# Kernel tuning notes

Hardware: AMD Instinct MI355X
Metric: run time of the kernel (lower is better)

## Reference

```python
import jax, jax.numpy as jnp
import numpy as np
from jax import lax

B, N, C = 16, 2000, 81
MAX_INST = 100
MIN_CONF = 0.7
NMS_THR = 0.3
BBOX_STD = jnp.array([0.1, 0.1, 0.2, 0.2], jnp.float32)
IMG_H = IMG_W = 1024
NEG = -1e9


def setup_inputs() -> dict:
    key = jax.random.key(0)
    k1, k2, k3 = jax.random.split(key, 3)
    # rois: normalized boxes with y1<y2, x1<x2
    yx = jax.random.uniform(k1, (B, N, 2, 2), dtype=jnp.float32)
    y = jnp.sort(yx[..., 0], axis=-1)
    x = jnp.sort(yx[..., 1], axis=-1)
    rois = jnp.stack([y[..., 0], x[..., 0], y[..., 1], x[..., 1]], axis=-1)
    # class probabilities (softmax over classes); temperature makes some scores pass 0.7
    mrcnn_class = jax.nn.softmax(3.0 * jax.random.normal(k2, (B, N, C), dtype=jnp.float32), axis=-1)
    mrcnn_bbox = 0.1 * jax.random.normal(k3, (B, N, C, 4), dtype=jnp.float32)
    # image_meta: [image_id(1), original_shape(3), image_shape(3), window(4), scale(1), active_class_ids(C)]
    meta = np.zeros((B, 12 + C), np.float32)
    meta[:, 1:4] = [IMG_H, IMG_W, 3]
    meta[:, 4:7] = [IMG_H, IMG_W, 3]
    meta[:, 7:11] = [0, 0, IMG_H, IMG_W]
    meta[:, 11] = 1.0
    return {"rois": rois, "mrcnn_class": mrcnn_class, "mrcnn_bbox": mrcnn_bbox,
            "image_meta": jnp.asarray(meta)}


def _apply_deltas(boxes, deltas):
    h = boxes[:, 2] - boxes[:, 0]
    w = boxes[:, 3] - boxes[:, 1]
    cy = boxes[:, 0] + 0.5 * h
    cx = boxes[:, 1] + 0.5 * w
    cy = cy + deltas[:, 0] * h
    cx = cx + deltas[:, 1] * w
    h = h * jnp.exp(deltas[:, 2])
    w = w * jnp.exp(deltas[:, 3])
    return jnp.stack([cy - 0.5 * h, cx - 0.5 * w, cy + 0.5 * h, cx + 0.5 * w], axis=-1)


def _iou_row(box, boxes):
    y1 = jnp.maximum(box[0], boxes[:, 0])
    x1 = jnp.maximum(box[1], boxes[:, 1])
    y2 = jnp.minimum(box[2], boxes[:, 2])
    x2 = jnp.minimum(box[3], boxes[:, 3])
    inter = jnp.maximum(y2 - y1, 0.0) * jnp.maximum(x2 - x1, 0.0)
    a1 = (box[2] - box[0]) * (box[3] - box[1])
    a2 = (boxes[:, 2] - boxes[:, 0]) * (boxes[:, 3] - boxes[:, 1])
    return inter / (a1 + a2 - inter + 1e-12)


def _refine_one(rois, probs, deltas, window):
    # rois [N,4], probs [N,C], deltas [N,C,4], window [4]
    idx = jnp.arange(N)
    class_ids = jnp.argmax(probs, axis=1)                 # [N]
    scores = probs[idx, class_ids]                        # [N]
    d = deltas[idx, class_ids] * BBOX_STD                 # [N,4]
    boxes = _apply_deltas(rois, d)
    wy1, wx1, wy2, wx2 = window[0], window[1], window[2], window[3]
    boxes = jnp.stack([jnp.clip(boxes[:, 0], wy1, wy2),
                       jnp.clip(boxes[:, 1], wx1, wx2),
                       jnp.clip(boxes[:, 2], wy1, wy2),
                       jnp.clip(boxes[:, 3], wx1, wx2)], axis=-1)
    # filter background and low confidence
    kept = (class_ids > 0) & (scores >= MIN_CONF)
    masked_scores = jnp.where(kept, scores, NEG)
    order = jnp.argsort(-masked_scores)                   # descending by score
    b = boxes[order]
    c = class_ids[order]
    s = masked_scores[order]
    suppressed0 = ~kept[order]

    def body(i, sup):
        iou = _iou_row(b[i], b)                           # [N]
        kill = (iou > NMS_THR) & (c == c[i]) & (idx > i) & (~sup[i])
        return sup | kill

    sup = lax.fori_loop(0, N, body, suppressed0)          # class-wise greedy NMS
    final = jnp.where(sup, NEG, s)
    top_s, top_i = lax.top_k(final, MAX_INST)             # global top detections
    det = jnp.concatenate([b[top_i],
                           c[top_i, None].astype(jnp.float32),
                           top_s[:, None]], axis=-1)      # [MAX_INST, 6]
    valid = top_s >= MIN_CONF
    return jnp.where(valid[:, None], det, 0.0)            # zero-pad invalid rows


def reference(rois, mrcnn_class, mrcnn_bbox, image_meta):
    image_shape = image_meta[0, 4:7]
    window = image_meta[:, 7:11]                          # [B,4] in pixels
    h, w = image_shape[0], image_shape[1]
    scale = jnp.stack([h - 1.0, w - 1.0, h - 1.0, w - 1.0])
    shift = jnp.array([0.0, 0.0, 1.0, 1.0], jnp.float32)
    norm_window = (window - shift) / scale                # norm_boxes_graph
    dets = jax.vmap(_refine_one)(rois, mrcnn_class, mrcnn_bbox, norm_window)
    return dets.reshape(B, MAX_INST, 6)
```

## Files before the change

### kernel.cpp

```cpp
#include <hip/hip_runtime.h>

#define NB    16
#define NN    2000
#define NC    81
#define NPAD  2048
#define MAXI  100
#define MINC  0.7f
#define NMST  0.3f
#define NEGV  -1000000000.0f
#define BTP   256
#define BT    1024
#define NWAVE (BT/64)
#define KQ    ((NN + BT - 1) / BT)

#define WS_BOX_OFF  0
#define WS_KEY_OFF  (NB * NN * 16)
#define WS_NEEDED   (WS_KEY_OFF + NB * NN * 8)

__device__ __forceinline__ unsigned ordf(float f) {
    unsigned u = __float_as_uint(f);
    return (u & 0x80000000u) ? ~u : (u | 0x80000000u);
}
__device__ __forceinline__ float unordf(unsigned u) {
    unsigned b = (u & 0x80000000u) ? (u ^ 0x80000000u) : ~u;
    return __uint_as_float(b);
}

__device__ __forceinline__ unsigned long long cx64(unsigned long long k, int j,
                                                   bool desc, int lane) {
    unsigned lo = __shfl_xor((unsigned)k, j, 64);
    unsigned hi = __shfl_xor((unsigned)(k >> 32), j, 64);
    unsigned long long p = ((unsigned long long)hi << 32) | lo;
    bool lower    = ((lane & j) == 0);
    bool take_max = (lower == desc);
    return ((p > k) == take_max) ? p : k;
}


__global__ __launch_bounds__(BTP)
void prep_kernel(const float* __restrict__ rois,
                 const float* __restrict__ probs,
                 const float* __restrict__ deltas,
                 const float* __restrict__ meta,
                 float4* __restrict__ wbox,
                 unsigned long long* __restrict__ wkey) {
    const int g = threadIdx.x >> 4;
    const int l = threadIdx.x & 15;
    const int r = blockIdx.x * 16 + g;
    const int b = r / NN;
    const int i = r - b * NN;

    const float* prow = probs + (size_t)r * NC;
    float best = -1.0f; int cb = 0;
    for (int c = l; c < NC; c += 16) {
        float p = prow[c];
        if (p > best) { best = p; cb = c; }
    }
    #pragma unroll
    for (int off = 8; off; off >>= 1) {
        float pb = __shfl_xor(best, off, 16);
        int   co = __shfl_xor(cb,   off, 16);
        if (pb > best || (pb == best && co < cb)) { best = pb; cb = co; }
    }

    if (l == 0) {
        const int MS = 12 + NC;
        const float ih = meta[4], iw = meta[5];
        const float sy = ih - 1.0f, sx = iw - 1.0f;
        const float wy1 = (meta[(size_t)b * MS + 7]        ) / sy;
        const float wx1 = (meta[(size_t)b * MS + 8]        ) / sx;
        const float wy2 = (meta[(size_t)b * MS + 9]  - 1.0f) / sy;
        const float wx2 = (meta[(size_t)b * MS + 10] - 1.0f) / sx;

        const float* drow = deltas + ((size_t)r * NC + cb) * 4;
        float dy = drow[0] * 0.1f, dx = drow[1] * 0.1f;
        float dh = drow[2] * 0.2f, dw = drow[3] * 0.2f;

        const float4 r4 = *(const float4*)(rois + (size_t)r * 4);
        float h  = r4.z - r4.x;
        float w  = r4.w - r4.y;
        float cy = r4.x + 0.5f * h;
        float cx = r4.y + 0.5f * w;
        cy = cy + dy * h;
        cx = cx + dx * w;
        h  = h * expf(dh);
        w  = w * expf(dw);
        float y1 = fminf(fmaxf(cy - 0.5f * h, wy1), wy2);
        float x1 = fminf(fmaxf(cx - 0.5f * w, wx1), wx2);
        float y2 = fminf(fmaxf(cy + 0.5f * h, wy1), wy2);
        float x2 = fminf(fmaxf(cx + 0.5f * w, wx1), wx2);

        wbox[r] = make_float4(y1, x1, y2, x2);
        bool kept = (cb > 0) && (best >= MINC);
        float msc = kept ? best : NEGV;
        wkey[r] = ((unsigned long long)ordf(msc) << 32)
                | (unsigned long long)(((unsigned)(2047 - i) << 8) | (unsigned)cb);
    }
}

__global__ __launch_bounds__(BT)
void det2_kernel(const float4* __restrict__ wbox,
                 const unsigned long long* __restrict__ wkey,
                 float* __restrict__ out) {
    __shared__ unsigned long long skey[NPAD];
    __shared__ float4 sboxR[NPAD];
    __shared__ unsigned char sup[NPAD];
    __shared__ unsigned short pool[NPAD];
    __shared__ int hist[82], cstart[82], cnt[82];
    __shared__ int out_rank[MAXI];
    __shared__ int sK, nsurv;

    const int b    = blockIdx.x;
    const int tid  = threadIdx.x;
    const int lane = tid & 63;
    const int wv   = tid >> 6;

    for (int c = tid; c < 82; c += BT) { hist[c] = 0; cnt[c] = 0; }
    if (tid == 0) { sK = 0; nsurv = 0; }
    __syncthreads();

    const unsigned minc_ord = ordf(MINC);
    unsigned long long kq[KQ];
    #pragma unroll
    for (int q = 0; q < KQ; ++q) {
        int i = q * BT + tid;
        kq[q] = (i < NN) ? wkey[(size_t)b * NN + i] : 0ull;
    }
    #pragma unroll
    for (int q = 0; q < KQ; ++q) {
        bool kept = ((unsigned)(kq[q] >> 32) >= minc_ord);
        unsigned long long m = __ballot(kept);
        int c64 = __popcll(m);
        int basep = 0;
        if (lane == 0 && c64) basep = atomicAdd(&sK, c64);
        basep = __shfl(basep, 0, 64);
        if (kept) skey[basep + __popcll(m & ((1ull << lane) - 1))] = kq[q];
    }
    __syncthreads();
    const int K = sK;
    int P = 0;
    if (K > 0) { P = 64; while (P < K) P <<= 1; }
    for (int t = K + tid; t < P; t += BT) skey[t] = 0ull;
    __syncthreads();

    if (P > 0 && P <= 64 * NWAVE) {
        const int nch = P >> 6;
        const int e   = (wv << 6) + lane;
        unsigned long long k = 0ull;
        if (wv < nch) {
            k = skey[e];
            #pragma unroll
            for (int kk2 = 2; kk2 <= 64; kk2 <<= 1) {
                #pragma unroll
                for (int j = 32; j; j >>= 1) {
                    if (j < kk2) k = cx64(k, j, ((e & kk2) == 0), lane);
                }
            }
            skey[e] = k;
        }
        __syncthreads();
        for (int kk = 128; kk <= P; kk <<= 1) {
            for (int j = kk >> 1; j >= 64; j >>= 1) {
                int jm = j - 1;
                for (int p = tid; p < (P >> 1); p += BT) {
                    int t  = ((p & ~jm) << 1) | (p & jm);
                    int ix = t + j;
                    unsigned long long a = skey[t], c2 = skey[ix];
                    bool desc = ((t & kk) == 0);
                    if ((a < c2) == desc) { skey[t] = c2; skey[ix] = a; }
                }
                __syncthreads();
            }
            if (wv < nch) {
                k = skey[e];
                const bool desc = ((e & kk) == 0);
                #pragma unroll
                for (int j = 32; j; j >>= 1) k = cx64(k, j, desc, lane);
                skey[e] = k;
            }
            __syncthreads();
        }
    } else if (P > 0) {
        for (int kk = 2; kk <= P; kk <<= 1) {
            for (int j = kk >> 1; j > 0; j >>= 1) {
                int jm = j - 1;
                for (int p = tid; p < (P >> 1); p += BT) {
                    int t  = ((p & ~jm) << 1) | (p & jm);
                    int ix = t + j;
                    unsigned long long a = skey[t], c2 = skey[ix];
                    bool desc = ((t & kk) == 0);
                    if ((a < c2) == desc) { skey[t] = c2; skey[ix] = a; }
                }
                __syncthreads();
            }
        }
    }

    for (int r2 = tid; r2 < K; r2 += BT) {
        unsigned low = (unsigned)(skey[r2] & 0xFFFFFFFFull);
        int oi = 2047 - (int)((low >> 8) & 0x7FF);
        sboxR[r2] = wbox[(size_t)b * NN + oi];
        sup[r2] = 0;
        atomicAdd(&hist[low & 0xFF], 1);
    }
    __syncthreads();

    if (wv == 0) {
        int c0 = 2 * lane, c1 = c0 + 1;
        int h0 = (c0 < 82) ? hist[c0] : 0;
        int h1 = (c1 < 82) ? hist[c1] : 0;
        int s = h0 + h1, sc = s;
        #pragma unroll
        for (int off = 1; off < 64; off <<= 1) {
            int v = __shfl_up(sc, off, 64);
            if (lane >= off) sc += v;
        }
        int excl = sc - s;
        if (c0 < 82) cstart[c0] = excl;
        if (c1 < 82) cstart[c1] = excl + h0;
    }
    __syncthreads();

    if (wv == 0) {
        for (int chunk = 0; chunk < K; chunk += 64) {
            int r2 = chunk + lane;
            bool v = r2 < K;
            int c = v ? (int)(skey[r2] & 0xFF) : 127;
            unsigned long long m = ~0ull;
            #pragma unroll
            for (int kb = 0; kb < 7; ++kb) {
                unsigned long long bk = __ballot((c >> kb) & 1);
                m &= ((c >> kb) & 1) ? bk : ~bk;
            }
            int leader = __ffsll(m) - 1;
            int before = __popcll(m & ((1ull << lane) - 1));
            int basec = 0;
            if (v && lane == leader) basec = atomicAdd(&cnt[c], __popcll(m));
            basec = __shfl(basec, leader, 64);
            if (v) pool[cstart[c] + basec + before] = (unsigned short)r2;
        }
    }
    __syncthreads();

    for (int c = 1 + wv; c < 82; c += NWAVE) {
        int s0 = cstart[c], n = hist[c];
        if (n <= 1) continue;
        if (n <= 64) {
            int ri = 0; float4 bi = make_float4(0.f,0.f,0.f,0.f);
            float ai = 0.f; bool alive = false;
            if (lane < n) {
                ri = pool[s0 + lane];
                bi = sboxR[ri];
                ai = (bi.z - bi.x) * (bi.w - bi.y);
                alive = true;
            }
            unsigned long long cand = __ballot(alive);
            while (cand) {
                int curl = __ffsll(cand) - 1;
                float cy1 = __shfl(bi.x, curl, 64);
                float cx1 = __shfl(bi.y, curl, 64);
                float cy2 = __shfl(bi.z, curl, 64);
                float cx2 = __shfl(bi.w, curl, 64);
                float ca  = __shfl(ai,  curl, 64);
                float yy1 = fmaxf(cy1, bi.x);
                float xx1 = fmaxf(cx1, bi.y);
                float yy2 = fminf(cy2, bi.z);
                float xx2 = fminf(cx2, bi.w);
                float inter = fmaxf(yy2 - yy1, 0.0f) * fmaxf(xx2 - xx1, 0.0f);
                float iou = inter / (ca + ai - inter + 1e-12f);
                bool kill = alive && (lane > curl) && (iou > NMST);
                unsigned long long km = __ballot(kill);
                if (kill) alive = false;
                cand &= ~km;
                cand &= ~(1ull << curl);
            }
            if (lane < n && !alive) sup[ri] = 1;
        } else {
            volatile unsigned char* vsup = sup;
            for (int ii = 0; ii < n; ++ii) {
                int ri = pool[s0 + ii];
                if (vsup[ri]) continue;
                float4 bi = sboxR[ri];
                float ai = (bi.z - bi.x) * (bi.w - bi.y);
                for (int jj = ii + 1 + lane; jj < n; jj += 64) {
                    int rj = pool[s0 + jj];
                    float4 bj = sboxR[rj];
                    float yy1 = fmaxf(bi.x, bj.x);
                    float xx1 = fmaxf(bi.y, bj.y);
                    float yy2 = fminf(bi.z, bj.z);
                    float xx2 = fminf(bi.w, bj.w);
                    float inter = fmaxf(yy2 - yy1, 0.0f) * fmaxf(xx2 - xx1, 0.0f);
                    float aj = (bj.z - bj.x) * (bj.w - bj.y);
                    float iou = inter / (ai + aj - inter + 1e-12f);
                    if (iou > NMST) vsup[rj] = 1;
                }
            }
        }
    }
    __syncthreads();

    if (wv == 0) {
        int total = 0;
        for (int chunk = 0; chunk < K && total < MAXI; chunk += 64) {
            int r2 = chunk + lane;
            bool alivex = (r2 < K) && !sup[r2];
            unsigned long long m = __ballot(alivex);
            int pos = total + __popcll(m & ((1ull << lane) - 1));
            if (alivex && pos < MAXI) out_rank[pos] = r2;
            total += __popcll(m);
        }
        if (lane == 0) nsurv = total < MAXI ? total : MAXI;
    }
    __syncthreads();

    const int ns = nsurv;
    for (int o = tid; o < MAXI; o += BT) {
        float v0=0.f,v1=0.f,v2=0.f,v3=0.f,v4=0.f,v5=0.f;
        if (o < ns) {
            int r2 = out_rank[o];
            float4 bo = sboxR[r2];
            unsigned long long kr = skey[r2];
            v0 = bo.x; v1 = bo.y; v2 = bo.z; v3 = bo.w;
            v4 = (float)(int)(kr & 0xFF);
            v5 = unordf((unsigned)(kr >> 32));
        }
        float* op = out + ((size_t)b * MAXI + o) * 6;
        op[0]=v0; op[1]=v1; op[2]=v2; op[3]=v3; op[4]=v4; op[5]=v5;
    }
}

__global__ __launch_bounds__(256)
void det_mono_kernel(const float* __restrict__ rois,
                     const float* __restrict__ probs,
                     const float* __restrict__ deltas,
                     const float* __restrict__ meta,
                     float* __restrict__ out) {
    __shared__ unsigned long long key[NPAD];
    __shared__ float4 sbox[NN];
    __shared__ unsigned char scls[NN];
    __shared__ unsigned char sup[NPAD];
    __shared__ int out_rank[MAXI];
    __shared__ int sK;
    __shared__ int nsurv;

    const int b   = blockIdx.x;
    const int tid = threadIdx.x;
    const int MSTRIDE = 12 + NC;

    if (tid == 0) { sK = 0; nsurv = 0; }

    const float ih = meta[4], iw = meta[5];
    const float sy = ih - 1.0f, sx = iw - 1.0f;
    const float wy1 = (meta[(size_t)b * MSTRIDE + 7]) / sy;
    const float wx1 = (meta[(size_t)b * MSTRIDE + 8]) / sx;
    const float wy2 = (meta[(size_t)b * MSTRIDE + 9] - 1.0f) / sy;
    const float wx2 = (meta[(size_t)b * MSTRIDE + 10] - 1.0f) / sx;

    for (int i = tid; i < NN; i += 256) {
        const float* prow = probs + ((size_t)b * NN + i) * NC;
        float best = prow[0];
        int cb = 0;
        #pragma unroll
        for (int c = 1; c < NC; ++c) {
            float p = prow[c];
            if (p > best) { best = p; cb = c; }
        }
        const float* drow = deltas + (((size_t)b * NN + i) * NC + cb) * 4;
        float dy = drow[0] * 0.1f, dx = drow[1] * 0.1f;
        float dh = drow[2] * 0.2f, dw = drow[3] * 0.2f;
        const float4 r4 = *(const float4*)(rois + ((size_t)b * NN + i) * 4);
        float h  = r4.z - r4.x;
        float w  = r4.w - r4.y;
        float cy = r4.x + 0.5f * h;
        float cx = r4.y + 0.5f * w;
        cy = cy + dy * h;
        cx = cx + dx * w;
        h  = h * expf(dh);
        w  = w * expf(dw);
        float y1 = fminf(fmaxf(cy - 0.5f * h, wy1), wy2);
        float x1 = fminf(fmaxf(cx - 0.5f * w, wx1), wx2);
        float y2 = fminf(fmaxf(cy + 0.5f * h, wy1), wy2);
        float x2 = fminf(fmaxf(cx + 0.5f * w, wx1), wx2);
        sbox[i] = make_float4(y1, x1, y2, x2);
        scls[i] = (unsigned char)cb;
        bool kept = (cb > 0) && (best >= MINC);
        float msc = kept ? best : NEGV;
        key[i] = ((unsigned long long)ordf(msc) << 32)
               | (unsigned long long)(0xFFFFFFFFu - (unsigned)i);
    }
    for (int i = NN + tid; i < NPAD; i += 256) key[i] = 0ull;
    __syncthreads();

    for (int k = 2; k <= NPAD; k <<= 1) {
        for (int j = k >> 1; j > 0; j >>= 1) {
            for (int t = tid; t < NPAD; t += 256) {
                int ix = t ^ j;
                if (ix > t) {
                    unsigned long long a = key[t], c = key[ix];
                    bool descend = ((t & k) == 0);
                    if ((a < c) == descend) { key[t] = c; key[ix] = a; }
                }
            }
            __syncthreads();
        }
    }

    const unsigned minc_ord = ordf(MINC);
    for (int r = tid; r < NPAD; r += 256) {
        unsigned su = (unsigned)(key[r] >> 32);
        bool kept = (su >= minc_ord);
        sup[r] = kept ? 0 : 1;
        if (kept) atomicAdd(&sK, 1);
    }
    __syncthreads();
    const int K = sK;

    for (int i = 0; i < K; ++i) {
        __syncthreads();
        if (nsurv >= MAXI) break;
        if (sup[i]) continue;
        unsigned long long ki = key[i];
        int oi = (int)(0xFFFFFFFFu - (unsigned)(ki & 0xFFFFFFFFull));
        float4 bi = sbox[oi];
        int ci = scls[oi];
        float ai = (bi.z - bi.x) * (bi.w - bi.y);
        for (int jr = i + 1 + tid; jr < K; jr += 256) {
            int oj = (int)(0xFFFFFFFFu - (unsigned)(key[jr] & 0xFFFFFFFFull));
            if ((int)scls[oj] != ci) continue;
            float4 bj = sbox[oj];
            float yy1 = fmaxf(bi.x, bj.x);
            float xx1 = fmaxf(bi.y, bj.y);
            float yy2 = fminf(bi.z, bj.z);
            float xx2 = fminf(bi.w, bj.w);
            float inter = fmaxf(yy2 - yy1, 0.0f) * fmaxf(xx2 - xx1, 0.0f);
            float aj = (bj.z - bj.x) * (bj.w - bj.y);
            float iou = inter / (ai + aj - inter + 1e-12f);
            if (iou > NMST) sup[jr] = 1;
        }
        if (tid == 0) { out_rank[nsurv] = i; nsurv += 1; }
    }
    __syncthreads();

    const int ns = nsurv;
    for (int o = tid; o < MAXI; o += 256) {
        float v0=0.f,v1=0.f,v2=0.f,v3=0.f,v4=0.f,v5=0.f;
        if (o < ns) {
            int r = out_rank[o];
            unsigned long long kr = key[r];
            int orr = (int)(0xFFFFFFFFu - (unsigned)(kr & 0xFFFFFFFFull));
            float4 bo = sbox[orr];
            v0 = bo.x; v1 = bo.y; v2 = bo.z; v3 = bo.w;
            v4 = (float)scls[orr];
            v5 = unordf((unsigned)(kr >> 32));
        }
        float* op = out + ((size_t)b * MAXI + o) * 6;
        op[0]=v0; op[1]=v1; op[2]=v2; op[3]=v3; op[4]=v4; op[5]=v5;
    }
}

extern "C" void kernel_launch(void* const* d_in, const int* in_sizes, int n_in,
                              void* d_out, int out_size, void* d_ws, size_t ws_size,
                              hipStream_t stream) {
    const float* rois   = (const float*)d_in[0];
    const float* probs  = (const float*)d_in[1];
    const float* deltas = (const float*)d_in[2];
    const float* meta   = (const float*)d_in[3];
    float* out = (float*)d_out;
    (void)in_sizes; (void)n_in; (void)out_size;

    if (ws_size >= (size_t)WS_NEEDED) {
        char* ws = (char*)d_ws;
        float4* wbox = (float4*)(ws + WS_BOX_OFF);
        unsigned long long* wkey = (unsigned long long*)(ws + WS_KEY_OFF);
        prep_kernel<<<(NB * NN) / 16, BTP, 0, stream>>>(rois, probs, deltas, meta,
                                                        wbox, wkey);
        det2_kernel<<<NB, BT, 0, stream>>>(wbox, wkey, out);
    } else {
        det_mono_kernel<<<NB, 256, 0, stream>>>(rois, probs, deltas, meta, out);
    }
}
```

Baseline: 25.52 us.

## Fuse per-ROI prep into the per-image detection kernel and drop workspace path

Moves the argmax, delta decoding and key building into the single per-image 1024-thread detection kernel, writing boxes and keys straight to shared memory. This removes the separate prep launch and the workspace round trip, and leaves sorting and NMS to index boxes by original ROI index. The cost is that the full ~10 MB class-probability read is now done by only 16 blocks instead of thousands spread across the GPU. That can make the kernel bound by memory latency and per-CU bandwidth. The fallback monolithic kernel is also deleted.

```diff
diff --git a/kernel.cpp b/kernel.cpp
--- a/kernel.cpp
+++ b/kernel.cpp
@@ -8,14 +8,8 @@
 #define MINC  0.7f
 #define NMST  0.3f
 #define NEGV  -1000000000.0f
-#define BTP   256
 #define BT    1024
 #define NWAVE (BT/64)
-#define KQ    ((NN + BT - 1) / BT)
-
-#define WS_BOX_OFF  0
-#define WS_KEY_OFF  (NB * NN * 16)
-#define WS_NEEDED   (WS_KEY_OFF + NB * NN * 8)
 
 __device__ __forceinline__ unsigned ordf(float f) {
     unsigned u = __float_as_uint(f);
@@ -37,73 +31,14 @@
 }
 
 
-__global__ __launch_bounds__(BTP)
-void prep_kernel(const float* __restrict__ rois,
-                 const float* __restrict__ probs,
-                 const float* __restrict__ deltas,
-                 const float* __restrict__ meta,
-                 float4* __restrict__ wbox,
-                 unsigned long long* __restrict__ wkey) {
-    const int g = threadIdx.x >> 4;
-    const int l = threadIdx.x & 15;
-    const int r = blockIdx.x * 16 + g;
-    const int b = r / NN;
-    const int i = r - b * NN;
-
-    const float* prow = probs + (size_t)r * NC;
-    float best = -1.0f; int cb = 0;
-    for (int c = l; c < NC; c += 16) {
-        float p = prow[c];
-        if (p > best) { best = p; cb = c; }
-    }
-    #pragma unroll
-    for (int off = 8; off; off >>= 1) {
-        float pb = __shfl_xor(best, off, 16);
-        int   co = __shfl_xor(cb,   off, 16);
-        if (pb > best || (pb == best && co < cb)) { best = pb; cb = co; }
-    }
-
-    if (l == 0) {
-        const int MS = 12 + NC;
-        const float ih = meta[4], iw = meta[5];
-        const float sy = ih - 1.0f, sx = iw - 1.0f;
-        const float wy1 = (meta[(size_t)b * MS + 7]        ) / sy;
-        const float wx1 = (meta[(size_t)b * MS + 8]        ) / sx;
-        const float wy2 = (meta[(size_t)b * MS + 9]  - 1.0f) / sy;
-        const float wx2 = (meta[(size_t)b * MS + 10] - 1.0f) / sx;
-
-        const float* drow = deltas + ((size_t)r * NC + cb) * 4;
-        float dy = drow[0] * 0.1f, dx = drow[1] * 0.1f;
-        float dh = drow[2] * 0.2f, dw = drow[3] * 0.2f;
-
-        const float4 r4 = *(const float4*)(rois + (size_t)r * 4);
-        float h  = r4.z - r4.x;
-        float w  = r4.w - r4.y;
-        float cy = r4.x + 0.5f * h;
-        float cx = r4.y + 0.5f * w;
-        cy = cy + dy * h;
-        cx = cx + dx * w;
-        h  = h * expf(dh);
-        w  = w * expf(dw);
-        float y1 = fminf(fmaxf(cy - 0.5f * h, wy1), wy2);
-        float x1 = fminf(fmaxf(cx - 0.5f * w, wx1), wx2);
-        float y2 = fminf(fmaxf(cy + 0.5f * h, wy1), wy2);
-        float x2 = fminf(fmaxf(cx + 0.5f * w, wx1), wx2);
-
-        wbox[r] = make_float4(y1, x1, y2, x2);
-        bool kept = (cb > 0) && (best >= MINC);
-        float msc = kept ? best : NEGV;
-        wkey[r] = ((unsigned long long)ordf(msc) << 32)
-                | (unsigned long long)(((unsigned)(2047 - i) << 8) | (unsigned)cb);
-    }
-}
-
 __global__ __launch_bounds__(BT)
-void det2_kernel(const float4* __restrict__ wbox,
-                 const unsigned long long* __restrict__ wkey,
-                 float* __restrict__ out) {
+void det_kernel(const float* __restrict__ rois,
+                const float* __restrict__ probs,
+                const float* __restrict__ deltas,
+                const float* __restrict__ meta,
+                float* __restrict__ out) {
     __shared__ unsigned long long skey[NPAD];
-    __shared__ float4 sboxR[NPAD];
+    __shared__ float4 sboxI[NN];
     __shared__ unsigned char sup[NPAD];
     __shared__ unsigned short pool[NPAD];
     __shared__ int hist[82], cstart[82], cnt[82];
@@ -117,17 +52,69 @@
 
     for (int c = tid; c < 82; c += BT) { hist[c] = 0; cnt[c] = 0; }
     if (tid == 0) { sK = 0; nsurv = 0; }
+
+    const int MS = 12 + NC;
+    const float ih = meta[4], iw = meta[5];
+    const float sy = ih - 1.0f, sx = iw - 1.0f;
+    const float wy1 = (meta[(size_t)b * MS + 7]        ) / sy;
+    const float wx1 = (meta[(size_t)b * MS + 8]        ) / sx;
+    const float wy2 = (meta[(size_t)b * MS + 9]  - 1.0f) / sy;
+    const float wx2 = (meta[(size_t)b * MS + 10] - 1.0f) / sx;
+
+    {
+        const int g = tid >> 4;
+        const int l = tid & 15;
+        for (int i = g; i < NN; i += 64) {
+            const size_t r = (size_t)b * NN + i;
+            const float* prow = probs + r * NC;
+            float best = -1.0f; int cb = 0;
+            for (int c = l; c < NC; c += 16) {
+                float p = prow[c];
+                if (p > best) { best = p; cb = c; }
+            }
+            #pragma unroll
+            for (int off = 8; off; off >>= 1) {
+                float pb = __shfl_xor(best, off, 16);
+                int   co = __shfl_xor(cb,   off, 16);
+                if (pb > best || (pb == best && co < cb)) { best = pb; cb = co; }
+            }
+            if (l == 0) {
+                const float* drow = deltas + (r * NC + cb) * 4;
+                float dy = drow[0] * 0.1f, dx = drow[1] * 0.1f;
+                float dh = drow[2] * 0.2f, dw = drow[3] * 0.2f;
+
+                const float4 r4 = *(const float4*)(rois + r * 4);
+                float h  = r4.z - r4.x;
+                float w  = r4.w - r4.y;
+                float cy = r4.x + 0.5f * h;
+                float cx = r4.y + 0.5f * w;
+                cy = cy + dy * h;
+                cx = cx + dx * w;
+                h  = h * expf(dh);
+                w  = w * expf(dw);
+                float y1 = fminf(fmaxf(cy - 0.5f * h, wy1), wy2);
+                float x1 = fminf(fmaxf(cx - 0.5f * w, wx1), wx2);
+                float y2 = fminf(fmaxf(cy + 0.5f * h, wy1), wy2);
+                float x2 = fminf(fmaxf(cx + 0.5f * w, wx1), wx2);
+
+                sboxI[i] = make_float4(y1, x1, y2, x2);
+                bool kept = (cb > 0) && (best >= MINC);
+                float msc = kept ? best : NEGV;
+                skey[i] = ((unsigned long long)ordf(msc) << 32)
+                        | (unsigned long long)(((unsigned)(2047 - i) << 8)
+                                               | (unsigned)cb);
+            }
+        }
+    }
     __syncthreads();
 
     const unsigned minc_ord = ordf(MINC);
-    unsigned long long kq[KQ];
+    unsigned long long kq[2];
+    kq[0] = skey[tid];
+    kq[1] = (BT + tid < NN) ? skey[BT + tid] : 0ull;
+    __syncthreads();
     #pragma unroll
-    for (int q = 0; q < KQ; ++q) {
-        int i = q * BT + tid;
-        kq[q] = (i < NN) ? wkey[(size_t)b * NN + i] : 0ull;
-    }
-    #pragma unroll
-    for (int q = 0; q < KQ; ++q) {
+    for (int q = 0; q < 2; ++q) {
         bool kept = ((unsigned)(kq[q] >> 32) >= minc_ord);
         unsigned long long m = __ballot(kept);
         int c64 = __popcll(m);
@@ -197,11 +184,8 @@
     }
 
     for (int r2 = tid; r2 < K; r2 += BT) {
-        unsigned low = (unsigned)(skey[r2] & 0xFFFFFFFFull);
-        int oi = 2047 - (int)((low >> 8) & 0x7FF);
-        sboxR[r2] = wbox[(size_t)b * NN + oi];
         sup[r2] = 0;
-        atomicAdd(&hist[low & 0xFF], 1);
+        atomicAdd(&hist[(int)(skey[r2] & 0xFF)], 1);
     }
     __syncthreads();
 
@@ -250,7 +234,8 @@
             float ai = 0.f; bool alive = false;
             if (lane < n) {
                 ri = pool[s0 + lane];
-                bi = sboxR[ri];
+                unsigned long long kr = skey[ri];
+                bi = sboxI[2047 - (int)(((unsigned)kr >> 8) & 0x7FF)];
                 ai = (bi.z - bi.x) * (bi.w - bi.y);
                 alive = true;
             }
@@ -280,11 +265,13 @@
             for (int ii = 0; ii < n; ++ii) {
                 int ri = pool[s0 + ii];
                 if (vsup[ri]) continue;
-                float4 bi = sboxR[ri];
+                unsigned long long kri = skey[ri];
+                float4 bi = sboxI[2047 - (int)(((unsigned)kri >> 8) & 0x7FF)];
                 float ai = (bi.z - bi.x) * (bi.w - bi.y);
                 for (int jj = ii + 1 + lane; jj < n; jj += 64) {
                     int rj = pool[s0 + jj];
-                    float4 bj = sboxR[rj];
+                    unsigned long long krj = skey[rj];
+                    float4 bj = sboxI[2047 - (int)(((unsigned)krj >> 8) & 0x7FF)];
                     float yy1 = fmaxf(bi.x, bj.x);
                     float xx1 = fmaxf(bi.y, bj.y);
                     float yy2 = fminf(bi.z, bj.z);
@@ -318,139 +305,10 @@
         float v0=0.f,v1=0.f,v2=0.f,v3=0.f,v4=0.f,v5=0.f;
         if (o < ns) {
             int r2 = out_rank[o];
-            float4 bo = sboxR[r2];
             unsigned long long kr = skey[r2];
+            float4 bo = sboxI[2047 - (int)(((unsigned)kr >> 8) & 0x7FF)];
             v0 = bo.x; v1 = bo.y; v2 = bo.z; v3 = bo.w;
             v4 = (float)(int)(kr & 0xFF);
-            v5 = unordf((unsigned)(kr >> 32));
-        }
-        float* op = out + ((size_t)b * MAXI + o) * 6;
-        op[0]=v0; op[1]=v1; op[2]=v2; op[3]=v3; op[4]=v4; op[5]=v5;
-    }
-}
-
-__global__ __launch_bounds__(256)
-void det_mono_kernel(const float* __restrict__ rois,
-                     const float* __restrict__ probs,
-                     const float* __restrict__ deltas,
-                     const float* __restrict__ meta,
-                     float* __restrict__ out) {
-    __shared__ unsigned long long key[NPAD];
-    __shared__ float4 sbox[NN];
-    __shared__ unsigned char scls[NN];
-    __shared__ unsigned char sup[NPAD];
-    __shared__ int out_rank[MAXI];
-    __shared__ int sK;
-    __shared__ int nsurv;
-
-    const int b   = blockIdx.x;
-    const int tid = threadIdx.x;
-    const int MSTRIDE = 12 + NC;
-
-    if (tid == 0) { sK = 0; nsurv = 0; }
-
-    const float ih = meta[4], iw = meta[5];
-    const float sy = ih - 1.0f, sx = iw - 1.0f;
-    const float wy1 = (meta[(size_t)b * MSTRIDE + 7]) / sy;
-    const float wx1 = (meta[(size_t)b * MSTRIDE + 8]) / sx;
-    const float wy2 = (meta[(size_t)b * MSTRIDE + 9] - 1.0f) / sy;
-    const float wx2 = (meta[(size_t)b * MSTRIDE + 10] - 1.0f) / sx;
-
-    for (int i = tid; i < NN; i += 256) {
-        const float* prow = probs + ((size_t)b * NN + i) * NC;
-        float best = prow[0];
-        int cb = 0;
-        #pragma unroll
-        for (int c = 1; c < NC; ++c) {
-            float p = prow[c];
-            if (p > best) { best = p; cb = c; }
-        }
-        const float* drow = deltas + (((size_t)b * NN + i) * NC + cb) * 4;
-        float dy = drow[0] * 0.1f, dx = drow[1] * 0.1f;
-        float dh = drow[2] * 0.2f, dw = drow[3] * 0.2f;
-        const float4 r4 = *(const float4*)(rois + ((size_t)b * NN + i) * 4);
-        float h  = r4.z - r4.x;
-        float w  = r4.w - r4.y;
-        float cy = r4.x + 0.5f * h;
-        float cx = r4.y + 0.5f * w;
-        cy = cy + dy * h;
-        cx = cx + dx * w;
-        h  = h * expf(dh);
-        w  = w * expf(dw);
-        float y1 = fminf(fmaxf(cy - 0.5f * h, wy1), wy2);
-        float x1 = fminf(fmaxf(cx - 0.5f * w, wx1), wx2);
-        float y2 = fminf(fmaxf(cy + 0.5f * h, wy1), wy2);
-        float x2 = fminf(fmaxf(cx + 0.5f * w, wx1), wx2);
-        sbox[i] = make_float4(y1, x1, y2, x2);
-        scls[i] = (unsigned char)cb;
-        bool kept = (cb > 0) && (best >= MINC);
-        float msc = kept ? best : NEGV;
-        key[i] = ((unsigned long long)ordf(msc) << 32)
-               | (unsigned long long)(0xFFFFFFFFu - (unsigned)i);
-    }
-    for (int i = NN + tid; i < NPAD; i += 256) key[i] = 0ull;
-    __syncthreads();
-
-    for (int k = 2; k <= NPAD; k <<= 1) {
-        for (int j = k >> 1; j > 0; j >>= 1) {
-            for (int t = tid; t < NPAD; t += 256) {
-                int ix = t ^ j;
-                if (ix > t) {
-                    unsigned long long a = key[t], c = key[ix];
-                    bool descend = ((t & k) == 0);
-                    if ((a < c) == descend) { key[t] = c; key[ix] = a; }
-                }
-            }
-            __syncthreads();
-        }
-    }
-
-    const unsigned minc_ord = ordf(MINC);
-    for (int r = tid; r < NPAD; r += 256) {
-        unsigned su = (unsigned)(key[r] >> 32);
-        bool kept = (su >= minc_ord);
-        sup[r] = kept ? 0 : 1;
-        if (kept) atomicAdd(&sK, 1);
-    }
-    __syncthreads();
-    const int K = sK;
-
-    for (int i = 0; i < K; ++i) {
-        __syncthreads();
-        if (nsurv >= MAXI) break;
-        if (sup[i]) continue;
-        unsigned long long ki = key[i];
-        int oi = (int)(0xFFFFFFFFu - (unsigned)(ki & 0xFFFFFFFFull));
-        float4 bi = sbox[oi];
-        int ci = scls[oi];
-        float ai = (bi.z - bi.x) * (bi.w - bi.y);
-        for (int jr = i + 1 + tid; jr < K; jr += 256) {
-            int oj = (int)(0xFFFFFFFFu - (unsigned)(key[jr] & 0xFFFFFFFFull));
-            if ((int)scls[oj] != ci) continue;
-            float4 bj = sbox[oj];
-            float yy1 = fmaxf(bi.x, bj.x);
-            float xx1 = fmaxf(bi.y, bj.y);
-            float yy2 = fminf(bi.z, bj.z);
-            float xx2 = fminf(bi.w, bj.w);
-            float inter = fmaxf(yy2 - yy1, 0.0f) * fmaxf(xx2 - xx1, 0.0f);
-            float aj = (bj.z - bj.x) * (bj.w - bj.y);
-            float iou = inter / (ai + aj - inter + 1e-12f);
-            if (iou > NMST) sup[jr] = 1;
-        }
-        if (tid == 0) { out_rank[nsurv] = i; nsurv += 1; }
-    }
-    __syncthreads();
-
-    const int ns = nsurv;
-    for (int o = tid; o < MAXI; o += 256) {
-        float v0=0.f,v1=0.f,v2=0.f,v3=0.f,v4=0.f,v5=0.f;
-        if (o < ns) {
-            int r = out_rank[o];
-            unsigned long long kr = key[r];
-            int orr = (int)(0xFFFFFFFFu - (unsigned)(kr & 0xFFFFFFFFull));
-            float4 bo = sbox[orr];
-            v0 = bo.x; v1 = bo.y; v2 = bo.z; v3 = bo.w;
-            v4 = (float)scls[orr];
             v5 = unordf((unsigned)(kr >> 32));
         }
         float* op = out + ((size_t)b * MAXI + o) * 6;
@@ -466,16 +324,7 @@
     const float* deltas = (const float*)d_in[2];
     const float* meta   = (const float*)d_in[3];
     float* out = (float*)d_out;
-    (void)in_sizes; (void)n_in; (void)out_size;
-
-    if (ws_size >= (size_t)WS_NEEDED) {
-        char* ws = (char*)d_ws;
-        float4* wbox = (float4*)(ws + WS_BOX_OFF);
-        unsigned long long* wkey = (unsigned long long*)(ws + WS_KEY_OFF);
-        prep_kernel<<<(NB * NN) / 16, BTP, 0, stream>>>(rois, probs, deltas, meta,
-                                                        wbox, wkey);
-        det2_kernel<<<NB, BT, 0, stream>>>(wbox, wkey, out);
-    } else {
-        det_mono_kernel<<<NB, 256, 0, stream>>>(rois, probs, deltas, meta, out);
-    }
-}
+    (void)in_sizes; (void)n_in; (void)out_size; (void)d_ws; (void)ws_size;
+
+    det_kernel<<<NB, BT, 0, stream>>>(rois, probs, deltas, meta, out);
+}
```

Result: slower. 62.37 us (+144.4%).

## Preload boxes by original index and overlap class histogram with sort

Applied to the files above, without the earlier changes.

Boxes are now loaded into shared memory indexed by original detection index, with a coalesced load at kernel start. This replaces the post-sort gather that used sorted ranks. The class histogram and sup reset move into the compaction step, and the prefix scan runs on an idle wave during the in-wave sort stage. Together these remove a full pass and a barrier after the sort. The cost is an extra indirection through skey on every box lookup, plus loading all 2000 boxes instead of only the kept ones.

```diff
diff --git a/kernel.cpp b/kernel.cpp
--- a/kernel.cpp
+++ b/kernel.cpp
@@ -11,7 +11,6 @@
 #define BTP   256
 #define BT    1024
 #define NWAVE (BT/64)
-#define KQ    ((NN + BT - 1) / BT)
 
 #define WS_BOX_OFF  0
 #define WS_KEY_OFF  (NB * NN * 16)
@@ -103,7 +102,7 @@
                  const unsigned long long* __restrict__ wkey,
                  float* __restrict__ out) {
     __shared__ unsigned long long skey[NPAD];
-    __shared__ float4 sboxR[NPAD];
+    __shared__ float4 sboxI[NN];
     __shared__ unsigned char sup[NPAD];
     __shared__ unsigned short pool[NPAD];
     __shared__ int hist[82], cstart[82], cnt[82];
@@ -120,21 +119,26 @@
     __syncthreads();
 
     const unsigned minc_ord = ordf(MINC);
-    unsigned long long kq[KQ];
+    unsigned long long kq[2];
+    kq[0] = wkey[(size_t)b * NN + tid];
+    kq[1] = (BT + tid < NN) ? wkey[(size_t)b * NN + BT + tid] : 0ull;
+    for (int i = tid; i < NN; i += BT)
+        sboxI[i] = wbox[(size_t)b * NN + i];
+
     #pragma unroll
-    for (int q = 0; q < KQ; ++q) {
-        int i = q * BT + tid;
-        kq[q] = (i < NN) ? wkey[(size_t)b * NN + i] : 0ull;
-    }
-    #pragma unroll
-    for (int q = 0; q < KQ; ++q) {
+    for (int q = 0; q < 2; ++q) {
         bool kept = ((unsigned)(kq[q] >> 32) >= minc_ord);
         unsigned long long m = __ballot(kept);
         int c64 = __popcll(m);
         int basep = 0;
         if (lane == 0 && c64) basep = atomicAdd(&sK, c64);
         basep = __shfl(basep, 0, 64);
-        if (kept) skey[basep + __popcll(m & ((1ull << lane) - 1))] = kq[q];
+        if (kept) {
+            int pos = basep + __popcll(m & ((1ull << lane) - 1));
+            skey[pos] = kq[q];
+            sup[pos] = 0;
+            atomicAdd(&hist[(int)(kq[q] & 0xFF)], 1);
+        }
     }
     __syncthreads();
     const int K = sK;
@@ -143,6 +147,7 @@
     for (int t = K + tid; t < P; t += BT) skey[t] = 0ull;
     __syncthreads();
 
+    bool prefixDone = false;
     if (P > 0 && P <= 64 * NWAVE) {
         const int nch = P >> 6;
         const int e   = (wv << 6) + lane;
@@ -157,7 +162,21 @@
                 }
             }
             skey[e] = k;
-        }
+        } else if (wv == nch) {
+            int c0 = 2 * lane, c1 = c0 + 1;
+            int h0 = (c0 < 82) ? hist[c0] : 0;
+            int h1 = (c1 < 82) ? hist[c1] : 0;
+            int s = h0 + h1, sc = s;
+            #pragma unroll
+            for (int off = 1; off < 64; off <<= 1) {
+                int v = __shfl_up(sc, off, 64);
+                if (lane >= off) sc += v;
+            }
+            int excl = sc - s;
+            if (c0 < 82) cstart[c0] = excl;
+            if (c1 < 82) cstart[c1] = excl + h0;
+        }
+        prefixDone = (nch < NWAVE);
         __syncthreads();
         for (int kk = 128; kk <= P; kk <<= 1) {
             for (int j = kk >> 1; j >= 64; j >>= 1) {
@@ -196,30 +215,23 @@
         }
     }
 
-    for (int r2 = tid; r2 < K; r2 += BT) {
-        unsigned low = (unsigned)(skey[r2] & 0xFFFFFFFFull);
-        int oi = 2047 - (int)((low >> 8) & 0x7FF);
-        sboxR[r2] = wbox[(size_t)b * NN + oi];
-        sup[r2] = 0;
-        atomicAdd(&hist[low & 0xFF], 1);
-    }
-    __syncthreads();
-
-    if (wv == 0) {
-        int c0 = 2 * lane, c1 = c0 + 1;
-        int h0 = (c0 < 82) ? hist[c0] : 0;
-        int h1 = (c1 < 82) ? hist[c1] : 0;
-        int s = h0 + h1, sc = s;
-        #pragma unroll
-        for (int off = 1; off < 64; off <<= 1) {
-            int v = __shfl_up(sc, off, 64);
-            if (lane >= off) sc += v;
-        }
-        int excl = sc - s;
-        if (c0 < 82) cstart[c0] = excl;
-        if (c1 < 82) cstart[c1] = excl + h0;
-    }
-    __syncthreads();
+    if (!prefixDone) {
+        if (wv == 0) {
+            int c0 = 2 * lane, c1 = c0 + 1;
+            int h0 = (c0 < 82) ? hist[c0] : 0;
+            int h1 = (c1 < 82) ? hist[c1] : 0;
+            int s = h0 + h1, sc = s;
+            #pragma unroll
+            for (int off = 1; off < 64; off <<= 1) {
+                int v = __shfl_up(sc, off, 64);
+                if (lane >= off) sc += v;
+            }
+            int excl = sc - s;
+            if (c0 < 82) cstart[c0] = excl;
+            if (c1 < 82) cstart[c1] = excl + h0;
+        }
+        __syncthreads();
+    }
 
     if (wv == 0) {
         for (int chunk = 0; chunk < K; chunk += 64) {
@@ -250,7 +262,8 @@
             float ai = 0.f; bool alive = false;
             if (lane < n) {
                 ri = pool[s0 + lane];
-                bi = sboxR[ri];
+                unsigned long long kr = skey[ri];
+                bi = sboxI[2047 - (int)(((unsigned)kr >> 8) & 0x7FF)];
                 ai = (bi.z - bi.x) * (bi.w - bi.y);
                 alive = true;
             }
@@ -280,11 +293,13 @@
             for (int ii = 0; ii < n; ++ii) {
                 int ri = pool[s0 + ii];
                 if (vsup[ri]) continue;
-                float4 bi = sboxR[ri];
+                unsigned long long kri = skey[ri];
+                float4 bi = sboxI[2047 - (int)(((unsigned)kri >> 8) & 0x7FF)];
                 float ai = (bi.z - bi.x) * (bi.w - bi.y);
                 for (int jj = ii + 1 + lane; jj < n; jj += 64) {
                     int rj = pool[s0 + jj];
-                    float4 bj = sboxR[rj];
+                    unsigned long long krj = skey[rj];
+                    float4 bj = sboxI[2047 - (int)(((unsigned)krj >> 8) & 0x7FF)];
                     float yy1 = fmaxf(bi.x, bj.x);
                     float xx1 = fmaxf(bi.y, bj.y);
                     float yy2 = fminf(bi.z, bj.z);
@@ -318,8 +333,8 @@
         float v0=0.f,v1=0.f,v2=0.f,v3=0.f,v4=0.f,v5=0.f;
         if (o < ns) {
             int r2 = out_rank[o];
-            float4 bo = sboxR[r2];
             unsigned long long kr = skey[r2];
+            float4 bo = sboxI[2047 - (int)(((unsigned)kr >> 8) & 0x7FF)];
             v0 = bo.x; v1 = bo.y; v2 = bo.z; v3 = bo.w;
             v4 = (float)(int)(kr & 0xFF);
             v5 = unordf((unsigned)(kr >> 32));
```

Result: no change. 25.59 us (+0.3%).
